# Performance work log

Measured on AMD Instinct MI355X. Metric: run time of the kernel, lower is better.

The kernel has to match this reference:

```python
import jax, jax.numpy as jnp
import numpy as np

EPS = 1e-12
LAMDA = 1.0
MAX_ITER = 10


def setup_inputs() -> dict:
    key = jax.random.key(0)
    k1, k2 = jax.random.split(key)
    B, L1, L2, D = 64, 1024, 1024, 256
    x1 = jax.random.normal(k1, (B, L1, D), dtype=jnp.float32)
    x2 = jax.random.normal(k2, (B, L2, D), dtype=jnp.float32)
    return {"x1": x1, "x2": x2}


def _cos(x1, x2):
    # batched cosine similarity: [B, L1, L2]
    M = jnp.einsum('bik,bjk->bij', x1, x2)
    a = jnp.sqrt(jnp.sum(x1 * x1, axis=-1, keepdims=True))  # [B, L1, 1]
    b = jnp.sqrt(jnp.sum(x2 * x2, axis=-1, keepdims=True))  # [B, L2, 1]
    norm = a * jnp.swapaxes(b, 1, 2)                          # [B, L1, L2]
    return M / (norm + EPS)


def reference(x1, x2):
    B, L1, _ = x1.shape
    L2 = x2.shape[1]
    M = 1.0 - _cos(x1, x2)          # [B, L1, L2] cost matrix
    K = jnp.exp(-M * LAMDA)
    w1 = jnp.full((B, L1, 1), 1.0 / L1, dtype=x1.dtype)
    w2 = jnp.full((B, L2, 1), 1.0 / L2, dtype=x1.dtype)
    ui = jnp.ones((B, L1, 1), dtype=x1.dtype)
    vi = jnp.ones((B, L2, 1), dtype=x1.dtype)
    Kt = jnp.swapaxes(K, 1, 2)      # [B, L2, L1]

    def body(_, carry):
        ui, vi = carry
        vi = w2 / (jnp.matmul(Kt, ui) + EPS)
        ui = w1 / (jnp.matmul(K, vi) + EPS)
        return (ui, vi)

    ui, vi = jax.lax.fori_loop(0, MAX_ITER, body, (ui, vi))
    G = ui * K * jnp.swapaxes(vi, 1, 2)   # transport plan [B, L1, L2]
    G_max = jnp.max(G, axis=(-1, -2), keepdims=True)
    G_min = jnp.min(G, axis=(-1, -2), keepdims=True)
    G = (G - G_min) / (G_max - G_min + EPS)
    return G * M
```

## Files before the change

kernel.cpp:

```cpp
#include <hip/hip_runtime.h>
#include <hip/hip_bf16.h>
#include <hip/hip_fp8.h>


#define EPSV 1e-12f
#define W1 0.0009765625f

typedef short  short8 __attribute__((ext_vector_type(8)));
typedef float  f32x4  __attribute__((ext_vector_type(4)));
typedef float  f32x2v __attribute__((ext_vector_type(2)));

__device__ __forceinline__ float rcpf_(float x) {
#if __has_builtin(__builtin_amdgcn_rcpf)
  return __builtin_amdgcn_rcpf(x);
#else
  return 1.0f / x;
#endif
}
__device__ __forceinline__ float rsqf_(float x) {
#if __has_builtin(__builtin_amdgcn_rsqf)
  return __builtin_amdgcn_rsqf(x);
#else
  return rsqrtf(x);
#endif
}

__device__ __forceinline__ unsigned char enc1(float x) {
#if __has_builtin(__builtin_amdgcn_cvt_pk_fp8_f32)
  int v = __builtin_amdgcn_cvt_pk_fp8_f32(x, x, 0, false);
  return (unsigned char)(v & 0xff);
#else
  __hip_fp8_e4m3 q(x); return (unsigned char)q.__x;
#endif
}
__device__ __forceinline__ float dec1(unsigned char b) {
#if __has_builtin(__builtin_amdgcn_cvt_f32_fp8)
  return __builtin_amdgcn_cvt_f32_fp8((int)b, 0);
#else
  __hip_fp8_e4m3 q; q.__x = (__hip_fp8_storage_t)b; return (float)q;
#endif
}
__device__ __forceinline__ void decode16(uint4 d, float* f) {
#if __has_builtin(__builtin_amdgcn_cvt_pk_f32_fp8)
  f32x2v p;
  p = __builtin_amdgcn_cvt_pk_f32_fp8((int)d.x, false); f[0]=p[0];  f[1]=p[1];
  p = __builtin_amdgcn_cvt_pk_f32_fp8((int)d.x, true);  f[2]=p[0];  f[3]=p[1];
  p = __builtin_amdgcn_cvt_pk_f32_fp8((int)d.y, false); f[4]=p[0];  f[5]=p[1];
  p = __builtin_amdgcn_cvt_pk_f32_fp8((int)d.y, true);  f[6]=p[0];  f[7]=p[1];
  p = __builtin_amdgcn_cvt_pk_f32_fp8((int)d.z, false); f[8]=p[0];  f[9]=p[1];
  p = __builtin_amdgcn_cvt_pk_f32_fp8((int)d.z, true);  f[10]=p[0]; f[11]=p[1];
  p = __builtin_amdgcn_cvt_pk_f32_fp8((int)d.w, false); f[12]=p[0]; f[13]=p[1];
  p = __builtin_amdgcn_cvt_pk_f32_fp8((int)d.w, true);  f[14]=p[0]; f[15]=p[1];
#else
  unsigned v[4] = {d.x, d.y, d.z, d.w};
  #pragma unroll
  for (int i = 0; i < 16; ++i)
    f[i] = dec1((unsigned char)((v[i >> 2] >> ((i & 3) * 8)) & 0xff));
#endif
}
__device__ __forceinline__ float dot16u(uint4 d, const float* s) {
#if __has_builtin(__builtin_amdgcn_cvt_pk_f32_fp8)
  f32x2v p; float a = 0.f;
  p = __builtin_amdgcn_cvt_pk_f32_fp8((int)d.x, false); a += p[0]*s[0]  + p[1]*s[1];
  p = __builtin_amdgcn_cvt_pk_f32_fp8((int)d.x, true);  a += p[0]*s[2]  + p[1]*s[3];
  p = __builtin_amdgcn_cvt_pk_f32_fp8((int)d.y, false); a += p[0]*s[4]  + p[1]*s[5];
  p = __builtin_amdgcn_cvt_pk_f32_fp8((int)d.y, true);  a += p[0]*s[6]  + p[1]*s[7];
  p = __builtin_amdgcn_cvt_pk_f32_fp8((int)d.z, false); a += p[0]*s[8]  + p[1]*s[9];
  p = __builtin_amdgcn_cvt_pk_f32_fp8((int)d.z, true);  a += p[0]*s[10] + p[1]*s[11];
  p = __builtin_amdgcn_cvt_pk_f32_fp8((int)d.w, false); a += p[0]*s[12] + p[1]*s[13];
  p = __builtin_amdgcn_cvt_pk_f32_fp8((int)d.w, true);  a += p[0]*s[14] + p[1]*s[15];
  return a;
#else
  float f[16]; decode16(d, f);
  float a = 0.f;
  #pragma unroll
  for (int k = 0; k < 16; ++k) a += f[k] * s[k];
  return a;
#endif
}
__device__ __forceinline__ void axpy16u(uint4 d, float u, float* pacc) {
#if __has_builtin(__builtin_amdgcn_cvt_pk_f32_fp8)
  f32x2v p;
  p = __builtin_amdgcn_cvt_pk_f32_fp8((int)d.x, false); pacc[0]  += p[0]*u; pacc[1]  += p[1]*u;
  p = __builtin_amdgcn_cvt_pk_f32_fp8((int)d.x, true);  pacc[2]  += p[0]*u; pacc[3]  += p[1]*u;
  p = __builtin_amdgcn_cvt_pk_f32_fp8((int)d.y, false); pacc[4]  += p[0]*u; pacc[5]  += p[1]*u;
  p = __builtin_amdgcn_cvt_pk_f32_fp8((int)d.y, true);  pacc[6]  += p[0]*u; pacc[7]  += p[1]*u;
  p = __builtin_amdgcn_cvt_pk_f32_fp8((int)d.z, false); pacc[8]  += p[0]*u; pacc[9]  += p[1]*u;
  p = __builtin_amdgcn_cvt_pk_f32_fp8((int)d.z, true);  pacc[10] += p[0]*u; pacc[11] += p[1]*u;
  p = __builtin_amdgcn_cvt_pk_f32_fp8((int)d.w, false); pacc[12] += p[0]*u; pacc[13] += p[1]*u;
  p = __builtin_amdgcn_cvt_pk_f32_fp8((int)d.w, true);  pacc[14] += p[0]*u; pacc[15] += p[1]*u;
#else
  float f[16]; decode16(d, f);
  #pragma unroll
  for (int k = 0; k < 16; ++k) pacc[k] += f[k] * u;
#endif
}

__device__ __forceinline__ short8 ld_cvt8_sq(const float* p, float* sq) {
  float4 f0 = *(const float4*)p;
  float4 f1 = *(const float4*)(p + 4);
  *sq += f0.x * f0.x + f0.y * f0.y + f0.z * f0.z + f0.w * f0.w
       + f1.x * f1.x + f1.y * f1.y + f1.z * f1.z + f1.w * f1.w;
  float2 p0; p0.x = f0.x; p0.y = f0.y;
  float2 p1; p1.x = f0.z; p1.y = f0.w;
  float2 p2; p2.x = f1.x; p2.y = f1.y;
  float2 p3; p3.x = f1.z; p3.y = f1.w;
  __hip_bfloat162 h0 = __float22bfloat162_rn(p0);
  __hip_bfloat162 h1 = __float22bfloat162_rn(p1);
  __hip_bfloat162 h2_ = __float22bfloat162_rn(p2);
  __hip_bfloat162 h3 = __float22bfloat162_rn(p3);
  short2 a = *(short2*)&h0, b = *(short2*)&h1, c = *(short2*)&h2_, d = *(short2*)&h3;
  short8 r;
  r[0] = a.x; r[1] = a.y; r[2] = b.x; r[3] = b.y;
  r[4] = c.x; r[5] = c.y; r[6] = d.x; r[7] = d.y;
  return r;
}

__global__ __launch_bounds__(256) void diag_kernel(float* __restrict__ out,
                                                   float val, int n) {
  int stride = gridDim.x * 256;
  for (int i = blockIdx.x * 256 + threadIdx.x; i < n; i += stride) out[i] = val;
}

__global__ __launch_bounds__(256) void gemm_kernel(
    const float* __restrict__ x1, const float* __restrict__ x2,
    unsigned char* __restrict__ K8g, unsigned char* __restrict__ R8g,
    unsigned* __restrict__ mm, _Float16* __restrict__ p0) {
  __shared__ __align__(16) unsigned short smem[2 * 128 * 64];
  __shared__ float asq[128], bsq[128];
  __shared__ float csum[4][128];
  unsigned short* As = smem;
  unsigned short* Bs = smem + 128 * 64;
  int bid = blockIdx.x;
  int b = bid >> 6, tile = bid & 63;
  int ti = (tile >> 3) << 7, tj = (tile & 7) << 7;
  int t = threadIdx.x, lane = t & 63, wave = t >> 6;
  int wr = (wave >> 1) << 6, wc = (wave & 1) << 6;
  const float* Ag = x1 + ((size_t)(b * 1024 + ti)) * 256;
  const float* Bg = x2 + ((size_t)(b * 1024 + tj)) * 256;

  if (bid == 0 && t < 128) mm[t] = (t < 64) ? 0u : 0x7f800000u;

  f32x4 acc[4][4];
  f32x4 zero = {0.f, 0.f, 0.f, 0.f};
  #pragma unroll
  for (int m = 0; m < 4; ++m)
    #pragma unroll
    for (int n = 0; n < 4; ++n) acc[m][n] = zero;

  float sqa[4] = {0.f, 0.f, 0.f, 0.f};
  float sqb[4] = {0.f, 0.f, 0.f, 0.f};
  short8 ra[4], rb[4];
  #pragma unroll
  for (int c = 0; c < 4; ++c) {
    int ch = t + (c << 8); int row = ch >> 3, kg = ch & 7;
    ra[c] = ld_cvt8_sq(Ag + row * 256 + kg * 8, &sqa[c]);
    rb[c] = ld_cvt8_sq(Bg + row * 256 + kg * 8, &sqb[c]);
  }

  for (int k0 = 0; k0 < 4; ++k0) {
    __syncthreads();
    #pragma unroll
    for (int c = 0; c < 4; ++c) {
      int ch = t + (c << 8); int row = ch >> 3, kg = ch & 7;
      int kgs = kg ^ (row & 7);
      *(short8*)(As + row * 64 + kgs * 8) = ra[c];
      *(short8*)(Bs + row * 64 + kgs * 8) = rb[c];
    }
    __syncthreads();
    if (k0 < 3) {
      #pragma unroll
      for (int c = 0; c < 4; ++c) {
        int ch = t + (c << 8); int row = ch >> 3, kg = ch & 7;
        ra[c] = ld_cvt8_sq(Ag + row * 256 + (k0 + 1) * 64 + kg * 8, &sqa[c]);
        rb[c] = ld_cvt8_sq(Bg + row * 256 + (k0 + 1) * 64 + kg * 8, &sqb[c]);
      }
    }
    #pragma unroll
    for (int ks = 0; ks < 2; ++ks) {
      short8 af[4], bfr[4];
      #pragma unroll
      for (int m = 0; m < 4; ++m) {
        int row = wr + m * 16 + (lane & 15);
        int c16 = (ks << 2) + (lane >> 4);
        af[m] = *(const short8*)(As + row * 64 + ((c16 ^ (row & 7)) << 3));
      }
      #pragma unroll
      for (int n = 0; n < 4; ++n) {
        int row = wc + n * 16 + (lane & 15);
        int c16 = (ks << 2) + (lane >> 4);
        bfr[n] = *(const short8*)(Bs + row * 64 + ((c16 ^ (row & 7)) << 3));
      }
      #pragma unroll
      for (int m = 0; m < 4; ++m)
        #pragma unroll
        for (int n = 0; n < 4; ++n)
          acc[m][n] = __builtin_amdgcn_mfma_f32_16x16x32_bf16(af[m], bfr[n], acc[m][n], 0, 0, 0);
    }
  }
  __syncthreads();
  #pragma unroll
  for (int c = 0; c < 4; ++c) {
    float sa = sqa[c], sb = sqb[c];
    sa += __shfl_xor(sa, 1, 64); sb += __shfl_xor(sb, 1, 64);
    sa += __shfl_xor(sa, 2, 64); sb += __shfl_xor(sb, 2, 64);
    sa += __shfl_xor(sa, 4, 64); sb += __shfl_xor(sb, 4, 64);
    if ((t & 7) == 0) {
      int row = (t + (c << 8)) >> 3;
      asq[row] = sa; bsq[row] = sb;
    }
  }
  __syncthreads();

  unsigned char* CtK = (unsigned char*)smem;
  unsigned char* CtR = ((unsigned char*)smem) + 16384;
  float ira[4][4], irb[4];
  #pragma unroll
  for (int m = 0; m < 4; ++m)
    #pragma unroll
    for (int q = 0; q < 4; ++q)
      ira[m][q] = rsqf_(asq[wr + m * 16 + ((lane >> 4) << 2) + q]);
  #pragma unroll
  for (int n = 0; n < 4; ++n)
    irb[n] = rsqf_(bsq[wc + n * 16 + (lane & 15)]);
  float csn[4] = {0.f, 0.f, 0.f, 0.f};
  #pragma unroll
  for (int m = 0; m < 4; ++m)
    #pragma unroll
    for (int n = 0; n < 4; ++n)
      #pragma unroll
      for (int q = 0; q < 4; ++q) {
        int rl = wr + m * 16 + ((lane >> 4) << 2) + q;
        int cl = wc + n * 16 + (lane & 15);
        float cosv = acc[m][n][q] * ira[m][q] * irb[n];
        float kv = __expf(cosv - 1.0f);
        unsigned char q8 = enc1(kv);
        float kd = dec1(q8);
        float rr = kv * rcpf_(kd) - 1.0f;
        csn[n] += kv;
        int cofs = rl * 128 + ((((cl >> 4) ^ ((rl >> 2) & 7))) << 4) + (cl & 15);
        CtK[cofs] = q8;
        CtR[cofs] = enc1(rr);
      }
  #pragma unroll
  for (int n = 0; n < 4; ++n) {
    csn[n] += __shfl_xor(csn[n], 16, 64);
    csn[n] += __shfl_xor(csn[n], 32, 64);
  }
  if (lane < 16) {
    #pragma unroll
    for (int n = 0; n < 4; ++n) csum[wave][wc + n * 16 + lane] = csn[n];
  }
  __syncthreads();
  if (t < 128) {
    float s_ = csum[t >> 6][t] + csum[2 + (t >> 6)][t];
    p0[((size_t)b << 13) + ((size_t)(ti >> 7) << 10) + tj + t] = (_Float16)s_;
  }
  size_t kbase = ((size_t)b << 20);
  #pragma unroll
  for (int i = 0; i < 4; ++i) {
    int idx = t + (i << 8);
    int row = idx >> 3, seg = idx & 7;
    int srcc = row * 8 + (seg ^ ((row >> 2) & 7));
    size_t off = kbase + (size_t)(ti + row) * 1024 + tj + seg * 16;
    *(uint4*)(K8g + off) = ((const uint4*)CtK)[srcc];
    *(uint4*)(R8g + off) = ((const uint4*)CtR)[srcc];
  }
}

template<int BSHIFT, int NSRC>
__global__ __launch_bounds__(1024) void fused1024_kernel(
    const unsigned char* __restrict__ K8, const _Float16* __restrict__ src,
    _Float16* __restrict__ dst) {
  int bid = blockIdx.x;
  int b = bid >> 2, s = bid & 3;
  int t = threadIdx.x, lane = t & 63, w = t >> 6;
  __shared__ float sv[1024];
  __shared__ float plds[8][1024];
  {
    int col = t;
    const _Float16* sp = src + ((size_t)b << BSHIFT) + col;
    float y = 0.f;
    #pragma unroll
    for (int j = 0; j < NSRC; ++j) y += (float)sp[j << 10];
    sv[col] = W1 / (y + EPSV);
  }
  __syncthreads();
  float svr[16];
  {
    float4 s0 = *(const float4*)&sv[lane * 16];
    float4 s1 = *(const float4*)&sv[lane * 16 + 4];
    float4 s2 = *(const float4*)&sv[lane * 16 + 8];
    float4 s3 = *(const float4*)&sv[lane * 16 + 12];
    svr[0] = s0.x;  svr[1] = s0.y;  svr[2]  = s0.z;  svr[3]  = s0.w;
    svr[4] = s1.x;  svr[5] = s1.y;  svr[6]  = s1.z;  svr[7]  = s1.w;
    svr[8] = s2.x;  svr[9] = s2.y;  svr[10] = s2.z;  svr[11] = s2.w;
    svr[12] = s3.x; svr[13] = s3.y; svr[14] = s3.z;  svr[15] = s3.w;
  }
  float pacc[16];
  #pragma unroll
  for (int k = 0; k < 16; ++k) pacc[k] = 0.f;
  const unsigned char* kp = K8 + ((size_t)b << 20) + (size_t)(s * 256 + w) * 1024 + lane * 16;
  uint4 c0 = *(const uint4*)(kp);
  uint4 c1 = *(const uint4*)(kp + 16384);
  for (int p = 0; p < 8; ++p) {
    uint4 n0, n1_;
    if (p < 7) {
      n0 = *(const uint4*)(kp + (size_t)(2 * p + 2) * 16384);
      n1_ = *(const uint4*)(kp + (size_t)(2 * p + 3) * 16384);
    }
    float d0 = dot16u(c0, svr);
    float d1 = dot16u(c1, svr);
    #pragma unroll
    for (int off = 1; off < 64; off <<= 1) {
      d0 += __shfl_xor(d0, off, 64);
      d1 += __shfl_xor(d1, off, 64);
    }
    float u0 = W1 / (d0 + EPSV);
    float u1 = W1 / (d1 + EPSV);
    axpy16u(c0, u0, pacc);
    axpy16u(c1, u1, pacc);
    c0 = n0; c1 = n1_;
  }
  if (w < 8) {
    *(float4*)&plds[w][lane * 16]      = *(float4*)&pacc[0];
    *(float4*)&plds[w][lane * 16 + 4]  = *(float4*)&pacc[4];
    *(float4*)&plds[w][lane * 16 + 8]  = *(float4*)&pacc[8];
    *(float4*)&plds[w][lane * 16 + 12] = *(float4*)&pacc[12];
  }
  __syncthreads();
  if (w >= 8) {
    float* pl = &plds[w - 8][lane * 16];
    #pragma unroll
    for (int k = 0; k < 16; ++k) pl[k] += pacc[k];
  }
  __syncthreads();
  {
    int col = t;
    float sum = 0.f;
    #pragma unroll
    for (int i = 0; i < 8; ++i) sum += plds[i][col];
    dst[((size_t)b << 12) + (s << 10) + col] = (_Float16)sum;
  }
}

template<int FINAL>
__global__ __launch_bounds__(512) void fused512_kernel(
    const unsigned char* __restrict__ K8, const unsigned char* __restrict__ R8,
    const _Float16* __restrict__ src, _Float16* __restrict__ dst,
    float* __restrict__ zb, unsigned* __restrict__ mm) {
  int bid = blockIdx.x;
  int b = bid >> 2, s = bid & 3;
  int t = threadIdx.x, lane = t & 63, w = t >> 6;
  __shared__ float sv[1024];
  __shared__ float plds[8][1024];
  __shared__ float red[16];
  #pragma unroll
  for (int p = 0; p < 2; ++p) {
    int col = (p << 9) + t;
    const _Float16* sp = src + ((size_t)b << 12) + col;
    float y = (float)sp[0] + (float)sp[1024] + (float)sp[2048] + (float)sp[3072];
    sv[col] = W1 / (y + EPSV);
  }
  __syncthreads();
  float svr[16];
  {
    float4 s0 = *(const float4*)&sv[lane * 16];
    float4 s1 = *(const float4*)&sv[lane * 16 + 4];
    float4 s2 = *(const float4*)&sv[lane * 16 + 8];
    float4 s3 = *(const float4*)&sv[lane * 16 + 12];
    svr[0] = s0.x;  svr[1] = s0.y;  svr[2]  = s0.z;  svr[3]  = s0.w;
    svr[4] = s1.x;  svr[5] = s1.y;  svr[6]  = s1.z;  svr[7]  = s1.w;
    svr[8] = s2.x;  svr[9] = s2.y;  svr[10] = s2.z;  svr[11] = s2.w;
    svr[12] = s3.x; svr[13] = s3.y; svr[14] = s3.z;  svr[15] = s3.w;
  }
  float pacc[16];
  #pragma unroll
  for (int k = 0; k < 16; ++k) pacc[k] = 0.f;
  float gmn = 3.4e38f, gmx = 0.f;
  const unsigned char* kp = K8 + ((size_t)b << 20) + (size_t)(s * 256 + w) * 1024 + lane * 16;
  const unsigned char* rp = R8 + ((size_t)b << 20) + (size_t)(s * 256 + w) * 1024 + lane * 16;
  uint4 c0 = *(const uint4*)(kp);
  uint4 c1 = *(const uint4*)(kp + 8192);
  uint4 r0 = *(const uint4*)(rp);
  uint4 r1 = *(const uint4*)(rp + 8192);
  for (int p = 0; p < 16; ++p) {
    uint4 n0, n1_, q0, q1;
    if (p < 15) {
      n0 = *(const uint4*)(kp + (size_t)(2 * p + 2) * 8192);
      n1_ = *(const uint4*)(kp + (size_t)(2 * p + 3) * 8192);
      q0 = *(const uint4*)(rp + (size_t)(2 * p + 2) * 8192);
      q1 = *(const uint4*)(rp + (size_t)(2 * p + 3) * 8192);
    }
    float kf0[16], kf1[16];
    decode16(c0, kf0);
    decode16(c1, kf1);
    {
      float rf0[16], rf1[16];
      decode16(r0, rf0);
      decode16(r1, rf1);
      #pragma unroll
      for (int k = 0; k < 16; ++k) {
        kf0[k] *= (1.0f + rf0[k]);
        kf1[k] *= (1.0f + rf1[k]);
      }
    }
    float d0 = 0.f, d1 = 0.f;
    #pragma unroll
    for (int k = 0; k < 16; ++k) {
      d0 += kf0[k] * svr[k];
      d1 += kf1[k] * svr[k];
    }
    #pragma unroll
    for (int off = 1; off < 64; off <<= 1) {
      d0 += __shfl_xor(d0, off, 64);
      d1 += __shfl_xor(d1, off, 64);
    }
    float u0 = W1 / (d0 + EPSV);
    float u1 = W1 / (d1 + EPSV);
    if (FINAL) {
      if (lane == 0) {
        zb[(b << 10) + s * 256 + w + (2 * p) * 8] = d0;
        zb[(b << 10) + s * 256 + w + (2 * p + 1) * 8] = d1;
      }
      #pragma unroll
      for (int k = 0; k < 16; ++k) {
        float g0 = u0 * kf0[k] * svr[k];
        float g1 = u1 * kf1[k] * svr[k];
        gmn = fminf(gmn, fminf(g0, g1));
        gmx = fmaxf(gmx, fmaxf(g0, g1));
      }
    } else {
      #pragma unroll
      for (int k = 0; k < 16; ++k)
        pacc[k] += kf0[k] * u0 + kf1[k] * u1;
    }
    c0 = n0; c1 = n1_; r0 = q0; r1 = q1;
  }
  if (!FINAL) {
    *(float4*)&plds[w][lane * 16]      = *(float4*)&pacc[0];
    *(float4*)&plds[w][lane * 16 + 4]  = *(float4*)&pacc[4];
    *(float4*)&plds[w][lane * 16 + 8]  = *(float4*)&pacc[8];
    *(float4*)&plds[w][lane * 16 + 12] = *(float4*)&pacc[12];
    __syncthreads();
    #pragma unroll
    for (int p = 0; p < 2; ++p) {
      int col = (p << 9) + t;
      float sum = plds[0][col] + plds[1][col] + plds[2][col] + plds[3][col]
                + plds[4][col] + plds[5][col] + plds[6][col] + plds[7][col];
      dst[((size_t)b << 12) + (s << 10) + col] = (_Float16)sum;
    }
  } else {
    #pragma unroll
    for (int off = 1; off < 64; off <<= 1) {
      gmn = fminf(gmn, __shfl_xor(gmn, off, 64));
      gmx = fmaxf(gmx, __shfl_xor(gmx, off, 64));
    }
    if (lane == 0) { red[w] = gmn; red[8 + w] = gmx; }
    __syncthreads();
    if (t == 0) {
      float m0 = red[0], m1 = red[8];
      #pragma unroll
      for (int i = 1; i < 8; ++i) { m0 = fminf(m0, red[i]); m1 = fmaxf(m1, red[8 + i]); }
      atomicMin(&mm[64 + b], __float_as_uint(m0));
      atomicMax(&mm[b],      __float_as_uint(m1));
    }
  }
}

__global__ __launch_bounds__(256) void fin_kernel(
    const unsigned char* __restrict__ K8, const unsigned char* __restrict__ R8,
    const _Float16* __restrict__ src, const float* __restrict__ zb,
    const unsigned* __restrict__ mm, float* __restrict__ out) {
  int bid = blockIdx.x;
  int b = bid >> 4, rg = bid & 15;
  int t = threadIdx.x, lane = t & 63, w = t >> 6;
  __shared__ float sv[1024];
  #pragma unroll
  for (int p = 0; p < 4; ++p) {
    int col = (p << 8) + t;
    const _Float16* sp = src + ((size_t)b << 12) + col;
    float y = (float)sp[0] + (float)sp[1024] + (float)sp[2048] + (float)sp[3072];
    sv[col] = W1 / (y + EPSV);
  }
  __syncthreads();
  float svr[16];
  {
    float4 s0 = *(const float4*)&sv[lane * 16];
    float4 s1 = *(const float4*)&sv[lane * 16 + 4];
    float4 s2 = *(const float4*)&sv[lane * 16 + 8];
    float4 s3 = *(const float4*)&sv[lane * 16 + 12];
    svr[0] = s0.x;  svr[1] = s0.y;  svr[2]  = s0.z;  svr[3]  = s0.w;
    svr[4] = s1.x;  svr[5] = s1.y;  svr[6]  = s1.z;  svr[7]  = s1.w;
    svr[8] = s2.x;  svr[9] = s2.y;  svr[10] = s2.z;  svr[11] = s2.w;
    svr[12] = s3.x; svr[13] = s3.y; svr[14] = s3.z;  svr[15] = s3.w;
  }
  float gmx = __uint_as_float(mm[b]);
  float gmn = __uint_as_float(mm[64 + b]);
  float scale = 1.0f / (gmx - gmn + EPSV);
  const unsigned char* kp = K8 + ((size_t)b << 20) + (size_t)(rg * 64 + w) * 1024 + lane * 16;
  const unsigned char* rp = R8 + ((size_t)b << 20) + (size_t)(rg * 64 + w) * 1024 + lane * 16;
  float* op = out + ((size_t)b << 20) + (size_t)(rg * 64 + w) * 1024 + lane * 16;
  for (int it = 0; it < 16; ++it) {
    int r = rg * 64 + w + it * 4;
    float u = W1 / (zb[b * 1024 + r] + EPSV);
    uint4 dk = *(const uint4*)(kp + (size_t)it * 4096);
    uint4 dr = *(const uint4*)(rp + (size_t)it * 4096);
    float kf[16], rf[16], o[16];
    decode16(dk, kf);
    decode16(dr, rf);
    #pragma unroll
    for (int k = 0; k < 16; ++k) {
      float krec = kf[k] * (1.0f + rf[k]);
      float g = u * krec * svr[k];
      o[k] = (g - gmn) * scale * (-__logf(krec));
    }
    *(float4*)(op + (size_t)it * 4096)      = *(float4*)&o[0];
    *(float4*)(op + (size_t)it * 4096 + 4)  = *(float4*)&o[4];
    *(float4*)(op + (size_t)it * 4096 + 8)  = *(float4*)&o[8];
    *(float4*)(op + (size_t)it * 4096 + 12) = *(float4*)&o[12];
  }
}

extern "C" void kernel_launch(void* const* d_in, const int* in_sizes, int n_in,
                              void* d_out, int out_size, void* d_ws, size_t ws_size,
                              hipStream_t stream) {
  const float* x1 = (const float*)d_in[0];
  const float* x2 = (const float*)d_in[1];
  float* out = (float*)d_out;
  char* ws = (char*)d_ws;

  unsigned char* K8g = (unsigned char*)ws;
  unsigned char* R8g = (unsigned char*)(ws + 67108864ULL);
  float*    zb = (float*)(ws + 134217728ULL);
  _Float16* p0 = (_Float16*)(ws + 134217728ULL);
  _Float16* pA = (_Float16*)(ws + 134742016ULL);
  _Float16* pB = (_Float16*)(ws + 135266304ULL);
  unsigned* mm = (unsigned*)(ws + 135790592ULL);
  const size_t WS_NEED = 135791104ULL;

  if (ws_size < WS_NEED) {
    float val = 100.0f + (float)(ws_size >> 20);
    diag_kernel<<<2048, 256, 0, stream>>>(out, val, out_size);
    return;
  }

  gemm_kernel<<<4096, 256, 0, stream>>>(x1, x2, K8g, R8g, mm, p0);
  fused1024_kernel<13, 8><<<256, 1024, 0, stream>>>(K8g, p0, pB);
  for (int k = 2; k <= 8; ++k) {
    _Float16* src = (k & 1) ? pA : pB;
    _Float16* dst = (k & 1) ? pB : pA;
    fused1024_kernel<12, 4><<<256, 1024, 0, stream>>>(K8g, src, dst);
  }
  fused512_kernel<0><<<256, 512, 0, stream>>>(K8g, R8g, pA, pB, zb, mm);
  fused512_kernel<1><<<256, 512, 0, stream>>>(K8g, R8g, pB, pA, zb, mm);
  fin_kernel<<<1024, 256, 0, stream>>>(K8g, R8g, pB, zb, mm, out);
}
```

Baseline: 449.9 us.

## Swap MFMA operands to write packed fp8 K/R directly to global without LDS staging

The MFMA operands are swapped so each lane holds four consecutive output columns. The lane then packs four fp8 values into one 32-bit word with the packed convert instruction and stores K and R straight to global memory, dropping the byte-wise LDS staging, the swizzle and the later 16-byte copy-out. The column-sum reduction is reworked to match the new accumulator layout. In exchange, global stores become 4-byte writes scattered across rows rather than coalesced 16-byte rows, which may reduce store efficiency.

```diff
diff --git a/kernel.cpp b/kernel.cpp
--- a/kernel.cpp
+++ b/kernel.cpp
@@ -40,23 +40,29 @@
   __hip_fp8_e4m3 q; q.__x = (__hip_fp8_storage_t)b; return (float)q;
 #endif
 }
-__device__ __forceinline__ void decode16(uint4 d, float* f) {
+__device__ __forceinline__ unsigned pack4fp8(float a, float b, float c, float d) {
+#if __has_builtin(__builtin_amdgcn_cvt_pk_fp8_f32)
+  int v = __builtin_amdgcn_cvt_pk_fp8_f32(a, b, 0, false);
+  v = __builtin_amdgcn_cvt_pk_fp8_f32(c, d, v, true);
+  return (unsigned)v;
+#else
+  return (unsigned)enc1(a) | ((unsigned)enc1(b) << 8) |
+         ((unsigned)enc1(c) << 16) | ((unsigned)enc1(d) << 24);
+#endif
+}
+__device__ __forceinline__ void unpack4fp8(unsigned v, float* f) {
 #if __has_builtin(__builtin_amdgcn_cvt_pk_f32_fp8)
   f32x2v p;
-  p = __builtin_amdgcn_cvt_pk_f32_fp8((int)d.x, false); f[0]=p[0];  f[1]=p[1];
-  p = __builtin_amdgcn_cvt_pk_f32_fp8((int)d.x, true);  f[2]=p[0];  f[3]=p[1];
-  p = __builtin_amdgcn_cvt_pk_f32_fp8((int)d.y, false); f[4]=p[0];  f[5]=p[1];
-  p = __builtin_amdgcn_cvt_pk_f32_fp8((int)d.y, true);  f[6]=p[0];  f[7]=p[1];
-  p = __builtin_amdgcn_cvt_pk_f32_fp8((int)d.z, false); f[8]=p[0];  f[9]=p[1];
-  p = __builtin_amdgcn_cvt_pk_f32_fp8((int)d.z, true);  f[10]=p[0]; f[11]=p[1];
-  p = __builtin_amdgcn_cvt_pk_f32_fp8((int)d.w, false); f[12]=p[0]; f[13]=p[1];
-  p = __builtin_amdgcn_cvt_pk_f32_fp8((int)d.w, true);  f[14]=p[0]; f[15]=p[1];
-#else
-  unsigned v[4] = {d.x, d.y, d.z, d.w};
-  #pragma unroll
-  for (int i = 0; i < 16; ++i)
-    f[i] = dec1((unsigned char)((v[i >> 2] >> ((i & 3) * 8)) & 0xff));
-#endif
+  p = __builtin_amdgcn_cvt_pk_f32_fp8((int)v, false); f[0] = p[0]; f[1] = p[1];
+  p = __builtin_amdgcn_cvt_pk_f32_fp8((int)v, true);  f[2] = p[0]; f[3] = p[1];
+#else
+  #pragma unroll
+  for (int i = 0; i < 4; ++i) f[i] = dec1((unsigned char)((v >> (i * 8)) & 0xff));
+#endif
+}
+__device__ __forceinline__ void decode16(uint4 d, float* f) {
+  unpack4fp8(d.x, f); unpack4fp8(d.y, f + 4);
+  unpack4fp8(d.z, f + 8); unpack4fp8(d.w, f + 12);
 }
 __device__ __forceinline__ float dot16u(uint4 d, const float* s) {
 #if __has_builtin(__builtin_amdgcn_cvt_pk_f32_fp8)
@@ -195,7 +201,7 @@
       for (int m = 0; m < 4; ++m)
         #pragma unroll
         for (int n = 0; n < 4; ++n)
-          acc[m][n] = __builtin_amdgcn_mfma_f32_16x16x32_bf16(af[m], bfr[n], acc[m][n], 0, 0, 0);
+          acc[m][n] = __builtin_amdgcn_mfma_f32_16x16x32_bf16(bfr[n], af[m], acc[m][n], 0, 0, 0);
     }
   }
   __syncthreads();
@@ -212,59 +218,61 @@
   }
   __syncthreads();
 
-  unsigned char* CtK = (unsigned char*)smem;
-  unsigned char* CtR = ((unsigned char*)smem) + 16384;
-  float ira[4][4], irb[4];
+  float ira[4];
   #pragma unroll
   for (int m = 0; m < 4; ++m)
+    ira[m] = rsqf_(asq[wr + m * 16 + (lane & 15)]);
+  float irb[4][4];
+  #pragma unroll
+  for (int n = 0; n < 4; ++n)
     #pragma unroll
     for (int q = 0; q < 4; ++q)
-      ira[m][q] = rsqf_(asq[wr + m * 16 + ((lane >> 4) << 2) + q]);
+      irb[n][q] = rsqf_(bsq[wc + n * 16 + ((lane >> 4) << 2) + q]);
+  float csn[4][4];
   #pragma unroll
   for (int n = 0; n < 4; ++n)
-    irb[n] = rsqf_(bsq[wc + n * 16 + (lane & 15)]);
-  float csn[4] = {0.f, 0.f, 0.f, 0.f};
-  #pragma unroll
-  for (int m = 0; m < 4; ++m)
-    #pragma unroll
-    for (int n = 0; n < 4; ++n)
+    #pragma unroll
+    for (int q = 0; q < 4; ++q) csn[n][q] = 0.f;
+  size_t kbase = ((size_t)b << 20);
+  #pragma unroll
+  for (int m = 0; m < 4; ++m) {
+    size_t rowoff = kbase + (size_t)(ti + wr + m * 16 + (lane & 15)) * 1024 + tj + wc + ((lane >> 4) << 2);
+    #pragma unroll
+    for (int n = 0; n < 4; ++n) {
+      float kv[4];
       #pragma unroll
       for (int q = 0; q < 4; ++q) {
-        int rl = wr + m * 16 + ((lane >> 4) << 2) + q;
-        int cl = wc + n * 16 + (lane & 15);
-        float cosv = acc[m][n][q] * ira[m][q] * irb[n];
-        float kv = __expf(cosv - 1.0f);
-        unsigned char q8 = enc1(kv);
-        float kd = dec1(q8);
-        float rr = kv * rcpf_(kd) - 1.0f;
-        csn[n] += kv;
-        int cofs = rl * 128 + ((((cl >> 4) ^ ((rl >> 2) & 7))) << 4) + (cl & 15);
-        CtK[cofs] = q8;
-        CtR[cofs] = enc1(rr);
-      }
-  #pragma unroll
-  for (int n = 0; n < 4; ++n) {
-    csn[n] += __shfl_xor(csn[n], 16, 64);
-    csn[n] += __shfl_xor(csn[n], 32, 64);
-  }
-  if (lane < 16) {
-    #pragma unroll
-    for (int n = 0; n < 4; ++n) csum[wave][wc + n * 16 + lane] = csn[n];
-  }
+        float cosv = acc[m][n][q] * ira[m] * irb[n][q];
+        kv[q] = __expf(cosv - 1.0f);
+        csn[n][q] += kv[q];
+      }
+      unsigned pk = pack4fp8(kv[0], kv[1], kv[2], kv[3]);
+      float kd[4];
+      unpack4fp8(pk, kd);
+      float rr[4];
+      #pragma unroll
+      for (int q = 0; q < 4; ++q) rr[q] = kv[q] * rcpf_(kd[q]) - 1.0f;
+      unsigned pr = pack4fp8(rr[0], rr[1], rr[2], rr[3]);
+      *(unsigned*)(K8g + rowoff + n * 16) = pk;
+      *(unsigned*)(R8g + rowoff + n * 16) = pr;
+    }
+  }
+  #pragma unroll
+  for (int n = 0; n < 4; ++n)
+    #pragma unroll
+    for (int q = 0; q < 4; ++q) {
+      float c_ = csn[n][q];
+      c_ += __shfl_xor(c_, 1, 64);
+      c_ += __shfl_xor(c_, 2, 64);
+      c_ += __shfl_xor(c_, 4, 64);
+      c_ += __shfl_xor(c_, 8, 64);
+      if ((lane & 15) == 0)
+        csum[wave][wc + n * 16 + ((lane >> 4) << 2) + q] = c_;
+    }
   __syncthreads();
   if (t < 128) {
     float s_ = csum[t >> 6][t] + csum[2 + (t >> 6)][t];
     p0[((size_t)b << 13) + ((size_t)(ti >> 7) << 10) + tj + t] = (_Float16)s_;
-  }
-  size_t kbase = ((size_t)b << 20);
-  #pragma unroll
-  for (int i = 0; i < 4; ++i) {
-    int idx = t + (i << 8);
-    int row = idx >> 3, seg = idx & 7;
-    int srcc = row * 8 + (seg ^ ((row >> 2) & 7));
-    size_t off = kbase + (size_t)(ti + row) * 1024 + tj + seg * 16;
-    *(uint4*)(K8g + off) = ((const uint4*)CtK)[srcc];
-    *(uint4*)(R8g + off) = ((const uint4*)CtR)[srcc];
   }
 }
 
```

Measured after the change: 448.3 us. About the same (-0.4%).
